# Kernel tuning notes

Measured on AMD Instinct MI355X. Metric: run time of the kernel, lower is better.

## Reference

```python
import jax, jax.numpy as jnp
import numpy as np

N_STATE = 2048
N_HEAD = 16
HEAD_DIM = N_STATE // N_HEAD  # 128
ROPE_THETA = 10000.0


def setup_inputs() -> dict:
    key = jax.random.key(0)
    ks = jax.random.split(key, 8)
    B, S, D = 2, 2048, N_STATE
    scale = 1.0 / np.sqrt(D)
    x = jax.random.normal(ks[0], (B, S, D), dtype=jnp.float32)
    Wq = jax.random.normal(ks[1], (D, D), dtype=jnp.float32) * scale
    bq = jnp.zeros((D,), dtype=jnp.float32)
    Wk = jax.random.normal(ks[2], (D, D), dtype=jnp.float32) * scale  # key has no bias
    Wv = jax.random.normal(ks[3], (D, D), dtype=jnp.float32) * scale
    bv = jnp.zeros((D,), dtype=jnp.float32)
    Wo = jax.random.normal(ks[4], (D, D), dtype=jnp.float32) * scale
    bo = jnp.zeros((D,), dtype=jnp.float32)
    return {"x": x, "Wq": Wq, "bq": bq, "Wk": Wk, "Wv": Wv, "bv": bv, "Wo": Wo, "bo": bo}


def _rope(t, pos):
    # t: [B, S, H, hd]; torchtune-style interleaved rotary (pairs of adjacent dims)
    hd = t.shape[-1]
    inv_freq = 1.0 / (ROPE_THETA ** (jnp.arange(0, hd, 2, dtype=jnp.float32) / hd))  # [hd/2]
    ang = pos[:, None] * inv_freq[None, :]                    # [S, hd/2]
    cos = jnp.cos(ang)[None, :, None, :].astype(t.dtype)       # [1,S,1,hd/2]
    sin = jnp.sin(ang)[None, :, None, :].astype(t.dtype)
    t1 = t[..., 0::2]
    t2 = t[..., 1::2]
    rot = jnp.stack([t1 * cos - t2 * sin, t2 * cos + t1 * sin], axis=-1)
    return rot.reshape(t.shape)


def reference(x, Wq, bq, Wk, Wv, bv, Wo, bo):
    B, S, D = x.shape
    H, hd = N_HEAD, D // N_HEAD
    q = (x @ Wq.T + bq).reshape(B, S, H, hd)
    k = (x @ Wk.T).reshape(B, S, H, hd)
    v = (x @ Wv.T + bv).reshape(B, S, H, hd)
    pos = jnp.arange(S, dtype=jnp.float32)
    q = _rope(q, pos)
    k = _rope(k, pos)
    # [B,H,S,hd]
    q = q.transpose(0, 2, 1, 3)
    k = k.transpose(0, 2, 1, 3)
    v = v.transpose(0, 2, 1, 3)
    scale = 1.0 / jnp.sqrt(jnp.asarray(hd, dtype=x.dtype))
    scores = jnp.einsum('bhqd,bhkd->bhqk', q, k) * scale       # [B,H,S,S]
    causal = jnp.tril(jnp.ones((S, S), dtype=bool))
    scores = jnp.where(causal[None, None], scores, jnp.finfo(scores.dtype).min)
    probs = jax.nn.softmax(scores, axis=-1)
    a = jnp.einsum('bhqk,bhkd->bhqd', probs, v)                # [B,H,S,hd]
    a = a.transpose(0, 2, 1, 3).reshape(B, S, D)
    return a @ Wo.T + bo
```

## Files before the change

### kernel.cpp

```cpp
#include <hip/hip_runtime.h>
#include <stdint.h>

typedef float f32x4 __attribute__((ext_vector_type(4)));
typedef __bf16 bf16x8 __attribute__((ext_vector_type(8)));
typedef unsigned short us8 __attribute__((ext_vector_type(8)));
typedef unsigned short us4 __attribute__((ext_vector_type(4)));
typedef unsigned int u32;

#define MFMA16(A, B, C) __builtin_amdgcn_mfma_f32_16x16x32_bf16( \
    __builtin_bit_cast(bf16x8, (A)), __builtin_bit_cast(bf16x8, (B)), (C), 0, 0, 0)

__device__ __forceinline__ unsigned short f2bf(float f) {
  u32 u = __builtin_bit_cast(u32, f);
  u = u + 0x7fffu + ((u >> 16) & 1u);
  return (unsigned short)(u >> 16);
}
__device__ __forceinline__ float bf2f(unsigned short b) {
  u32 u = ((u32)b) << 16;
  return __builtin_bit_cast(float, u);
}
__device__ __forceinline__ void gload16(const void* g, void* lds) {
  __builtin_amdgcn_global_load_lds((const __attribute__((address_space(1))) u32*)g,
                                   (__attribute__((address_space(3))) u32*)lds, 16, 0, 0);
}

__global__ __launch_bounds__(256) void convert_all(
    const float* __restrict__ x, const float* __restrict__ wq, const float* __restrict__ wk,
    const float* __restrict__ wv, const float* __restrict__ wo,
    unsigned short* __restrict__ xb, unsigned short* __restrict__ wcat,
    unsigned short* __restrict__ wob, float2* __restrict__ tab) {
  if (blockIdx.x >= 2048) {
    int t0 = ((int)blockIdx.x - 2048) * 2048 + (int)threadIdx.x * 8;
#pragma unroll
    for (int j = 0; j < 8; ++j) {
      int idx = t0 + j;
      int s = idx >> 6, i = idx & 63;
      float ang = (float)s * exp2f(-(float)i * 0.2076205059304703f);
      float sv, cv;
      sincosf(ang, &sv, &cv);
      tab[idx] = make_float2(cv, sv);
    }
    return;
  }
  int tid = blockIdx.x * 256 + threadIdx.x;
  int nth = 2048 * 256;
  const float* srcs[5] = {x, wq, wk, wv, wo};
  unsigned short* dsts[5] = {xb, wcat, wcat + 4194304, wcat + 8388608, wob};
  const int n4s[5] = {2097152, 1048576, 1048576, 1048576, 1048576};
#pragma unroll
  for (int sg = 0; sg < 5; ++sg) {
    const float4* s = (const float4*)srcs[sg];
    us4* d = (us4*)dsts[sg];
    int n4 = n4s[sg];
    for (int i = tid; i < n4; i += nth) {
      float4 v = s[i];
      us4 o;
      o[0] = f2bf(v.x); o[1] = f2bf(v.y); o[2] = f2bf(v.z); o[3] = f2bf(v.w);
      d[i] = o;
    }
  }
}

template <int EPI>
__global__ __launch_bounds__(512, 2) void gemmsw(
    const unsigned short* __restrict__ A, const unsigned short* __restrict__ B,
    int nTN, int N,
    float* __restrict__ outF, const float* __restrict__ bias,
    unsigned short* __restrict__ qb, unsigned short* __restrict__ kb,
    unsigned short* __restrict__ vtb, const float* __restrict__ bq,
    const float* __restrict__ bv, const float2* __restrict__ tab) {
  constexpr int KT = 32;
  __shared__ alignas(16) char L[131072];
  char* Lp = L;
  int bid = (int)blockIdx.x, nwg = (int)gridDim.x;
  {
    int qq = nwg >> 3;
    int xcd = bid & 7, idx = bid >> 3;
    bid = xcd * qq + idx;
  }
  int tm = bid / nTN, tn = bid % nTN;
  int t = (int)threadIdx.x, l = t & 63, w = t >> 6;
  int g = l >> 4, ln = l & 15;
  int wr = w >> 2, wc = w & 3;
  int lr = l >> 3, lc = l & 7;
  int scol = lc ^ lr;
  const unsigned short* pAs = A + (size_t)(tm * 256 + w * 8 + lr) * 2048 + scol * 8;
  const unsigned short* pBs = B + (size_t)(tn * 256 + w * 8 + lr) * 2048 + scol * 8;

  f32x4 acc[2][2][4][2] = {};
  us8 af[4][2], bf[2][2][2];

#define FENCE asm volatile("" ::: "memory")
#define BAR do { FENCE; __builtin_amdgcn_s_barrier(); FENCE; } while (0)
#define VMW_(n) asm volatile("s_waitcnt vmcnt(" #n ")" ::: "memory")
#define VMW(n) VMW_(n)
#define STA(i, kt, bufsel) do { if ((kt) < KT)                                \
    gload16(pAs + (size_t)(i) * 131072 + (size_t)(kt) * 64,                   \
            Lp + (bufsel) * 65536 + (i) * 8192 + w * 1024); } while (0)
#define STB(i, kt, bufsel) do { if ((kt) < KT)                                \
    gload16(pBs + (size_t)(i) * 131072 + (size_t)(kt) * 64,                   \
            Lp + (bufsel) * 65536 + 32768 + (i) * 8192 + w * 1024); } while (0)
#define RD_A(mh_, bufsel) do {                                                \
    _Pragma("unroll") for (int mf = 0; mf < 4; ++mf)                          \
    _Pragma("unroll") for (int kc = 0; kc < 2; ++kc)                          \
      af[mf][kc] = *(const us8*)(Lp + (bufsel) * 65536 +                      \
          (wr * 128 + (mh_) * 64 + mf * 16 + ln) * 128 +                      \
          ((kc * 64 + g * 16) ^ ((ln & 7) << 4)));                            \
  } while (0)
#define RD_B(nh_, bufsel) do {                                                \
    _Pragma("unroll") for (int nf = 0; nf < 2; ++nf)                          \
    _Pragma("unroll") for (int kc = 0; kc < 2; ++kc)                          \
      bf[nh_][nf][kc] = *(const us8*)(Lp + (bufsel) * 65536 + 32768 +         \
          (wc * 64 + (nh_) * 32 + nf * 16 + ln) * 128 +                       \
          ((kc * 64 + g * 16) ^ ((ln & 7) << 4)));                            \
  } while (0)
#define MM(mh_, nh_) do {                                                     \
    __builtin_amdgcn_s_setprio(1);                                            \
    _Pragma("unroll") for (int mf = 0; mf < 4; ++mf)                          \
    _Pragma("unroll") for (int nf = 0; nf < 2; ++nf)                          \
    _Pragma("unroll") for (int kc = 0; kc < 2; ++kc)                          \
      acc[mh_][nh_][mf][nf] = MFMA16(af[mf][kc], bf[nh_][nf][kc],             \
                                     acc[mh_][nh_][mf][nf]);                  \
    __builtin_amdgcn_s_setprio(0);                                            \
  } while (0)
#define TILE(kt, b, VM0, VM1, VM3) do {                                       \
   RD_A(0, b); RD_B(0, b);                                             \
          STB(0, (kt) + 1, (b) ^ 1); STB(1, (kt) + 1, (b) ^ 1);               \
          BAR; MM(0, 0); VMW(VM0); BAR;                                       \
   RD_B(1, b);                                                         \
          STA(0, (kt) + 1, (b) ^ 1); STA(2, (kt) + 1, (b) ^ 1);               \
          BAR; MM(0, 1); VMW(VM1); BAR;                                       \
   RD_A(1, b);                                                         \
          STB(2, (kt) + 1, (b) ^ 1); STB(3, (kt) + 1, (b) ^ 1);               \
          BAR; MM(1, 0); BAR;                                                 \
   STA(1, (kt) + 1, (b) ^ 1); STA(3, (kt) + 1, (b) ^ 1);               \
          MM(1, 1); VMW(VM3); BAR;                                            \
} while (0)

  STB(0, 0, 0); STB(1, 0, 0); STA(0, 0, 0); STA(2, 0, 0);
  STB(2, 0, 0); STB(3, 0, 0); STA(1, 0, 0); STA(3, 0, 0);
  VMW(4); BAR;

#pragma unroll 1
  for (int kt = 0; kt < 30; kt += 2) {
    TILE(kt, 0, 4, 4, 4);
    TILE(kt + 1, 1, 4, 4, 4);
  }
  TILE(30, 0, 4, 4, 4);
  TILE(31, 1, 2, 0, 0);

#undef TILE
#undef MM
#undef RD_B
#undef RD_A
#undef STB
#undef STA
#undef VMW
#undef VMW_
#undef BAR
#undef FENCE

  if (EPI == 1) {
#pragma unroll
    for (int mh = 0; mh < 2; ++mh)
#pragma unroll
    for (int nh = 0; nh < 2; ++nh)
#pragma unroll
    for (int mf = 0; mf < 4; ++mf)
#pragma unroll
    for (int nf = 0; nf < 2; ++nf) {
      int n = tn * 256 + wc * 64 + nh * 32 + nf * 16 + ln;
      float bz = bias[n];
      int m0 = tm * 256 + wr * 128 + mh * 64 + mf * 16 + g * 4;
#pragma unroll
      for (int r = 0; r < 4; ++r)
        outF[(size_t)(m0 + r) * N + n] = acc[mh][nh][mf][nf][r] + bz;
    }
  } else {
#pragma unroll
    for (int mh = 0; mh < 2; ++mh)
#pragma unroll
    for (int nh = 0; nh < 2; ++nh)
#pragma unroll
    for (int mf = 0; mf < 4; ++mf)
#pragma unroll
    for (int nf = 0; nf < 2; ++nf) {
      int n6 = tn * 256 + wc * 64 + nh * 32 + nf * 16 + ln;
      int sel = n6 >> 11, d = n6 & 2047, h = d >> 7, hd = d & 127;
      int m0 = tm * 256 + wr * 128 + mh * 64 + mf * 16 + g * 4;
      int b = m0 >> 11, s0 = m0 & 2047;
      if (sel == 2) {
        float badd = bv[d];
        us4 pk;
#pragma unroll
        for (int r = 0; r < 4; ++r) pk[r] = f2bf(acc[mh][nh][mf][nf][r] + badd);
        *(us4*)&vtb[((size_t)(b * 16 + h) * 128 + hd) * 2048 + s0] = pk;
      } else {
        unsigned short* dst = sel ? kb : qb;
        float badd = sel ? 0.f : bq[d];
        int odd = hd & 1;
#pragma unroll
        for (int r = 0; r < 4; ++r) {
          float val = acc[mh][nh][mf][nf][r] + badd;
          float pv = __shfl_xor(val, 1);
          float2 cs = tab[((s0 + r) << 6) | (hd >> 1)];
          float rot = odd ? (val * cs.x + pv * cs.y) : (val * cs.x - pv * cs.y);
          dst[((size_t)(b * 16 + h) * 2048 + (s0 + r)) * 128 + hd] = f2bf(rot);
        }
      }
    }
  }
}

template <int EPI>
__global__ __launch_bounds__(512, 2) void gemm2(
    const unsigned short* __restrict__ A, const unsigned short* __restrict__ B,
    int nTN, int N,
    float* __restrict__ outF, const float* __restrict__ bias) {
  constexpr int K = 2048, KT = 64;
  __shared__ alignas(16) char L[4 * 24576];
  int bid = (int)blockIdx.x, nwg = (int)gridDim.x;
  {
    int qq = nwg >> 3;
    int xcd = bid & 7, idx = bid >> 3;
    bid = xcd * qq + idx;
  }
  int tm = bid / nTN, tn = bid % nTN;
  int t = (int)threadIdx.x, l = t & 63, w = t >> 6;
  int g = l >> 4, ln = l & 15;
  int wr = w >> 2, wc = w & 3;
  const unsigned short* Ab =
      A + (size_t)(tm * 128 + w * 16 + (l >> 2)) * K + (((l & 3) ^ ((l >> 4) & 3))) * 8;
  const unsigned short* Bb =
      B + (size_t)(tn * 256 + w * 16 + (l >> 2)) * K + (((l & 3) ^ ((l >> 4) & 3))) * 8;
  f32x4 acc[4][4] = {};

#define STAGE(tile) do {                                                      \
    char* Lb = L + ((tile) & 3) * 24576 + w * 1024;                           \
    int kc = (tile) * 32;                                                     \
    gload16(Ab + kc, Lb);                                                     \
    gload16(Bb + kc, Lb + 8192);                                              \
    gload16(Bb + (size_t)128 * K + kc, Lb + 16384);                           \
  } while (0)

#define GITER(kt, VM) do {                                                    \
    asm volatile("s_waitcnt vmcnt(" #VM ")" ::: "memory");                    \
    __builtin_amdgcn_s_barrier();                                             \
    __builtin_amdgcn_sched_barrier(0);                                        \
    asm volatile("" ::: "memory");                                            \
    if ((kt) + 3 < KT) STAGE((kt) + 3);                                       \
    const unsigned short* Lc = (const unsigned short*)(L + ((kt) & 3) * 24576); \
    us8 af[4], bfr[4];                                                        \
    _Pragma("unroll") for (int mf = 0; mf < 4; ++mf)                          \
      af[mf] = *(const us8*)&Lc[(wr * 64 + mf * 16 + ln) * 32 +               \
                                ((g ^ ((ln >> 2) & 3)) * 8)];                 \
    _Pragma("unroll") for (int nf = 0; nf < 4; ++nf)                          \
      bfr[nf] = *(const us8*)&Lc[4096 + (wc * 64 + nf * 16 + ln) * 32 +       \
                                 ((g ^ ((ln >> 2) & 3)) * 8)];                \
    __builtin_amdgcn_s_setprio(1);                                            \
    _Pragma("unroll") for (int mf = 0; mf < 4; ++mf)                          \
      _Pragma("unroll") for (int nf = 0; nf < 4; ++nf)                        \
        acc[mf][nf] = MFMA16(af[mf], bfr[nf], acc[mf][nf]);                   \
    __builtin_amdgcn_s_setprio(0);                                            \
  } while (0)

  STAGE(0); STAGE(1); STAGE(2);
#pragma unroll 1
  for (int kt = 0; kt < KT - 2; ++kt) GITER(kt, 6);
  GITER(KT - 2, 3);
  GITER(KT - 1, 0);
#undef STAGE
#undef GITER

#pragma unroll
  for (int mf = 0; mf < 4; ++mf)
#pragma unroll
    for (int nf = 0; nf < 4; ++nf) {
      int n = tn * 256 + wc * 64 + nf * 16 + ln;
      float bz = bias[n];
#pragma unroll
      for (int r = 0; r < 4; ++r) {
        int m = tm * 128 + wr * 64 + mf * 16 + g * 4 + r;
        outF[(size_t)m * N + n] = acc[mf][nf][r] + bz;
      }
    }
}

__global__ __launch_bounds__(512) void attn_k(
    const unsigned short* __restrict__ qg, const unsigned short* __restrict__ kg,
    const unsigned short* __restrict__ vtg, unsigned short* __restrict__ ab) {
  __shared__ alignas(16) unsigned short Kl[2][64 * 128];
  __shared__ alignas(16) unsigned short Vl[2][128 * 64];
  __shared__ alignas(16) unsigned short Pl[8][16 * 72];
  int bh = (int)blockIdx.x & 31;
  int pr = (int)blockIdx.x >> 5;
  int t = (int)threadIdx.x, l = t & 63, w = t >> 6;
  int g = l >> 4, ln = l & 15;
  int b = bh >> 4, h = bh & 15;
  const size_t bq0 = (size_t)bh * 2048 * 128;

  const int qbA = pr * 128, qbB = (15 - pr) * 128;
  const int qrowA = qbA + w * 16 + ln, qrowB = qbB + w * 16 + ln;
  us8 qfA[4], qfB[4];
#pragma unroll
  for (int kf = 0; kf < 4; ++kf) {
    qfA[kf] = *(const us8*)&qg[bq0 + (size_t)qrowA * 128 + kf * 32 + g * 8];
    qfB[kf] = *(const us8*)&qg[bq0 + (size_t)qrowB * 128 + kf * 32 + g * 8];
  }
  f32x4 oA[8] = {}, oB[8] = {};
  float mA = -1e30f, lA = 0.f, mB = -1e30f, lB = 0.f;
  const int nktA = (qbA >> 6) + 2;
  const int nkt  = (qbB >> 6) + 2;

#define STAGEKV(kt1, bsel) do {                                               \
    _Pragma("unroll") for (int i = 0; i < 2; ++i) {                           \
      int fb = i * 8192 + w * 1024;                                           \
      int flat = fb + l * 16;                                                 \
      int row = flat >> 8, colb = flat & 255;                                 \
      int sc = colb ^ ((row & 7) << 4);                                       \
      gload16(kg + (bq0 + (size_t)((kt1) * 64 + row) * 128 + (sc >> 1)),      \
              (char*)Kl + (bsel) * 16384 + fb);                               \
      int rv = flat >> 7, cv2 = flat & 127;                                   \
      int scv = cv2 ^ ((rv & 7) << 4);                                        \
      gload16(vtg + (bq0 + (size_t)rv * 2048 + (kt1) * 64 + (scv >> 1)),      \
              (char*)Vl + (bsel) * 16384 + fb);                               \
    }                                                                         \
  } while (0)

#define COMPUTE(qf, o, mrow, lrow, qrow, kt, bo) do {                         \
    f32x4 st[4];                                                              \
    _Pragma("unroll") for (int kfr = 0; kfr < 4; ++kfr) {                     \
      f32x4 acc = {};                                                         \
      int row = kfr * 16 + ln;                                                \
      int swz = (row & 7) << 4;                                               \
      _Pragma("unroll") for (int kf = 0; kf < 4; ++kf) {                      \
        us8 kfrag = *(const us8*)((const char*)Kl + (bo) + row * 256 +        \
                                  ((kf * 64 + g * 16) ^ swz));                \
        acc = MFMA16(kfrag, qf[kf], acc);                                     \
      }                                                                       \
      st[kfr] = acc;                                                          \
    }                                                                         \
    float pmax = -1e30f;                                                      \
    _Pragma("unroll") for (int kfr = 0; kfr < 4; ++kfr)                       \
    _Pragma("unroll") for (int r = 0; r < 4; ++r) {                           \
      int key = (kt) * 64 + kfr * 16 + g * 4 + r;                             \
      float sv = key <= (qrow) ? st[kfr][r] * 0.08838834764831845f : -1e30f;  \
      st[kfr][r] = sv;                                                        \
      pmax = fmaxf(pmax, sv);                                                 \
    }                                                                         \
    pmax = fmaxf(pmax, __shfl_xor(pmax, 16));                                 \
    pmax = fmaxf(pmax, __shfl_xor(pmax, 32));                                 \
    if (__ballot(pmax > (mrow) + 8.f)) {                                      \
      float mnew = pmax > (mrow) + 8.f ? pmax : (mrow);                       \
      float corr = exp2f(((mrow) - mnew) * 1.44269504f);                      \
      (mrow) = mnew;                                                          \
      (lrow) *= corr;                                                         \
      _Pragma("unroll") for (int r = 0; r < 4; ++r) {                         \
        float cr = __shfl(corr, g * 4 + r);                                   \
        _Pragma("unroll") for (int nf = 0; nf < 8; ++nf) o[nf][r] *= cr;      \
      }                                                                       \
    }                                                                         \
    float lsum = 0.f;                                                         \
    _Pragma("unroll") for (int kfr = 0; kfr < 4; ++kfr) {                     \
      us4 pk;                                                                 \
      _Pragma("unroll") for (int r = 0; r < 4; ++r) {                         \
        float p = exp2f((st[kfr][r] - (mrow)) * 1.44269504f);                 \
        lsum += p;                                                            \
        pk[r] = f2bf(p);                                                      \
      }                                                                       \
      *(us4*)&Pl[w][ln * 72 + kfr * 16 + g * 4] = pk;                         \
    }                                                                         \
    lsum += __shfl_xor(lsum, 16);                                             \
    lsum += __shfl_xor(lsum, 32);                                             \
    (lrow) += lsum;                                                           \
    _Pragma("unroll") for (int kf2 = 0; kf2 < 2; ++kf2) {                     \
      us8 pa = *(const us8*)&Pl[w][ln * 72 + kf2 * 32 + g * 8];               \
      _Pragma("unroll") for (int nf = 0; nf < 8; ++nf) {                      \
        int row = nf * 16 + ln;                                               \
        us8 vb = *(const us8*)((const char*)Vl + (bo) + row * 128 +           \
                               ((kf2 * 64 + g * 16) ^ ((row & 7) << 4)));     \
        o[nf] = MFMA16(pa, vb, o[nf]);                                        \
      }                                                                       \
    }                                                                         \
  } while (0)

  STAGEKV(0, 0);
#pragma unroll 1
  for (int kt = 0; kt < nkt; ++kt) {
    __syncthreads();
    if (kt + 1 < nkt) STAGEKV(kt + 1, (kt + 1) & 1);
    int bo = (kt & 1) * 16384;
    COMPUTE(qfB, oB, mB, lB, qrowB, kt, bo);
    if (kt < nktA) COMPUTE(qfA, oA, mA, lA, qrowA, kt, bo);
  }
#undef COMPUTE
#undef STAGEKV

  {
    float invl = 1.f / lB;
#pragma unroll
    for (int r = 0; r < 4; ++r) {
      float ir = __shfl(invl, g * 4 + r);
      int srow = qbB + w * 16 + g * 4 + r;
      size_t base = ((size_t)b * 2048 + srow) * 2048 + h * 128 + ln;
#pragma unroll
      for (int nf = 0; nf < 8; ++nf) ab[base + (size_t)nf * 16] = f2bf(oB[nf][r] * ir);
    }
  }
  {
    float invl = 1.f / lA;
#pragma unroll
    for (int r = 0; r < 4; ++r) {
      float ir = __shfl(invl, g * 4 + r);
      int srow = qbA + w * 16 + g * 4 + r;
      size_t base = ((size_t)b * 2048 + srow) * 2048 + h * 128 + ln;
#pragma unroll
      for (int nf = 0; nf < 8; ++nf) ab[base + (size_t)nf * 16] = f2bf(oA[nf][r] * ir);
    }
  }
}

extern "C" void kernel_launch(void* const* d_in, const int* in_sizes, int n_in,
                              void* d_out, int out_size, void* d_ws, size_t ws_size,
                              hipStream_t stream) {
  const float* x  = (const float*)d_in[0];
  const float* Wq = (const float*)d_in[1];
  const float* bq = (const float*)d_in[2];
  const float* Wk = (const float*)d_in[3];
  const float* Wv = (const float*)d_in[4];
  const float* bv = (const float*)d_in[5];
  const float* Wo = (const float*)d_in[6];
  const float* bo = (const float*)d_in[7];
  float* out = (float*)d_out;

  unsigned short* ws = (unsigned short*)d_ws;
  unsigned short* xb   = ws;
  unsigned short* wcat = xb + 8388608;
  unsigned short* wob  = wcat + 12582912;
  unsigned short* qb   = wob + 4194304;
  unsigned short* kb   = qb + 8388608;
  unsigned short* vtb  = kb + 8388608;
  float2* tab = (float2*)(vtb + 8388608);

  convert_all<<<2112, 256, 0, stream>>>(x, Wq, Wk, Wv, Wo, xb, wcat, wob, tab);
  gemmsw<0><<<384, 512, 0, stream>>>(xb, wcat, 24, 6144,
                                     nullptr, nullptr, qb, kb, vtb, bq, bv, tab);
  attn_k<<<256, 512, 0, stream>>>(qb, kb, vtb, xb );
  gemm2<1><<<256, 512, 0, stream>>>(xb, wob, 8, 2048, out, bo);
}
```

Measured before the change: 266.3 us.

## Retile QKV projection GEMM to 256x192 tiles with 512 workgroups

The fused QKV GEMM tile changes from 256x256 to 256x192. The grid grows from 384 to 512 workgroups, which divides evenly across the 256 CUs instead of leaving a partial second wave, and LDS per block drops to 112KB. The inner loop is restructured: all A fragments are loaded once per k-tile, then three N-slices are streamed through with a new load/barrier/waitcnt schedule. The trade-off is lower arithmetic intensity per tile, more total A traffic, and a hand-tuned vmcnt schedule that must stay correct.

```diff
diff --git a/kernel.cpp b/kernel.cpp
--- a/kernel.cpp
+++ b/kernel.cpp
@@ -70,7 +70,7 @@
     unsigned short* __restrict__ vtb, const float* __restrict__ bq,
     const float* __restrict__ bv, const float2* __restrict__ tab) {
   constexpr int KT = 32;
-  __shared__ alignas(16) char L[131072];
+  __shared__ alignas(16) char L[114688];
   char* Lp = L;
   int bid = (int)blockIdx.x, nwg = (int)gridDim.x;
   {
@@ -85,10 +85,10 @@
   int lr = l >> 3, lc = l & 7;
   int scol = lc ^ lr;
   const unsigned short* pAs = A + (size_t)(tm * 256 + w * 8 + lr) * 2048 + scol * 8;
-  const unsigned short* pBs = B + (size_t)(tn * 256 + w * 8 + lr) * 2048 + scol * 8;
-
-  f32x4 acc[2][2][4][2] = {};
-  us8 af[4][2], bf[2][2][2];
+  const unsigned short* pBs = B + (size_t)(tn * 192 + w * 8 + lr) * 2048 + scol * 8;
+
+  f32x4 acc[2][3][4] = {};
+  us8 af[2][4][2], bf[2];
 
 #define FENCE asm volatile("" ::: "memory")
 #define BAR do { FENCE; __builtin_amdgcn_s_barrier(); FENCE; } while (0)
@@ -96,63 +96,62 @@
 #define VMW(n) VMW_(n)
 #define STA(i, kt, bufsel) do { if ((kt) < KT)                                \
     gload16(pAs + (size_t)(i) * 131072 + (size_t)(kt) * 64,                   \
-            Lp + (bufsel) * 65536 + (i) * 8192 + w * 1024); } while (0)
+            Lp + (bufsel) * 57344 + (i) * 8192 + w * 1024); } while (0)
 #define STB(i, kt, bufsel) do { if ((kt) < KT)                                \
     gload16(pBs + (size_t)(i) * 131072 + (size_t)(kt) * 64,                   \
-            Lp + (bufsel) * 65536 + 32768 + (i) * 8192 + w * 1024); } while (0)
-#define RD_A(mh_, bufsel) do {                                                \
+            Lp + (bufsel) * 57344 + 32768 + (i) * 8192 + w * 1024); } while (0)
+#define RD_AALL(bufsel) do {                                                  \
+    _Pragma("unroll") for (int mh = 0; mh < 2; ++mh)                          \
     _Pragma("unroll") for (int mf = 0; mf < 4; ++mf)                          \
     _Pragma("unroll") for (int kc = 0; kc < 2; ++kc)                          \
-      af[mf][kc] = *(const us8*)(Lp + (bufsel) * 65536 +                      \
-          (wr * 128 + (mh_) * 64 + mf * 16 + ln) * 128 +                      \
+      af[mh][mf][kc] = *(const us8*)(Lp + (bufsel) * 57344 +                  \
+          (wr * 128 + mh * 64 + mf * 16 + ln) * 128 +                         \
           ((kc * 64 + g * 16) ^ ((ln & 7) << 4)));                            \
   } while (0)
 #define RD_B(nh_, bufsel) do {                                                \
-    _Pragma("unroll") for (int nf = 0; nf < 2; ++nf)                          \
     _Pragma("unroll") for (int kc = 0; kc < 2; ++kc)                          \
-      bf[nh_][nf][kc] = *(const us8*)(Lp + (bufsel) * 65536 + 32768 +         \
-          (wc * 64 + (nh_) * 32 + nf * 16 + ln) * 128 +                       \
+      bf[kc] = *(const us8*)(Lp + (bufsel) * 57344 + 32768 +                  \
+          ((nh_) * 64 + wc * 16 + ln) * 128 +                                 \
           ((kc * 64 + g * 16) ^ ((ln & 7) << 4)));                            \
   } while (0)
-#define MM(mh_, nh_) do {                                                     \
+#define MMF(nh_) do {                                                         \
     __builtin_amdgcn_s_setprio(1);                                            \
+    _Pragma("unroll") for (int kc = 0; kc < 2; ++kc)                          \
+    _Pragma("unroll") for (int mh = 0; mh < 2; ++mh)                          \
     _Pragma("unroll") for (int mf = 0; mf < 4; ++mf)                          \
-    _Pragma("unroll") for (int nf = 0; nf < 2; ++nf)                          \
-    _Pragma("unroll") for (int kc = 0; kc < 2; ++kc)                          \
-      acc[mh_][nh_][mf][nf] = MFMA16(af[mf][kc], bf[nh_][nf][kc],             \
-                                     acc[mh_][nh_][mf][nf]);                  \
+      acc[mh][nh_][mf] = MFMA16(af[mh][mf][kc], bf[kc], acc[mh][nh_][mf]);    \
     __builtin_amdgcn_s_setprio(0);                                            \
   } while (0)
-#define TILE(kt, b, VM0, VM1, VM3) do {                                       \
-   RD_A(0, b); RD_B(0, b);                                             \
-          STB(0, (kt) + 1, (b) ^ 1); STB(1, (kt) + 1, (b) ^ 1);               \
-          BAR; MM(0, 0); VMW(VM0); BAR;                                       \
+#define TILE(kt, b, VM0, VM1, VMB) do {                                       \
+   RD_AALL(b); RD_B(0, b);                                             \
+          STA(0, (kt) + 1, (b) ^ 1); STA(1, (kt) + 1, (b) ^ 1);               \
+          STA(2, (kt) + 1, (b) ^ 1); STA(3, (kt) + 1, (b) ^ 1);               \
+          STB(0, (kt) + 1, (b) ^ 1);                                          \
+          BAR; MMF(0); VMW(VM0); BAR;                                         \
    RD_B(1, b);                                                         \
-          STA(0, (kt) + 1, (b) ^ 1); STA(2, (kt) + 1, (b) ^ 1);               \
-          BAR; MM(0, 1); VMW(VM1); BAR;                                       \
-   RD_A(1, b);                                                         \
-          STB(2, (kt) + 1, (b) ^ 1); STB(3, (kt) + 1, (b) ^ 1);               \
-          BAR; MM(1, 0); BAR;                                                 \
-   STA(1, (kt) + 1, (b) ^ 1); STA(3, (kt) + 1, (b) ^ 1);               \
-          MM(1, 1); VMW(VM3); BAR;                                            \
+          STB(1, (kt) + 1, (b) ^ 1);                                          \
+          BAR; MMF(1); VMW(VM1); BAR;                                         \
+   RD_B(2, b);                                                         \
+          STB(2, (kt) + 1, (b) ^ 1);                                          \
+          MMF(2); VMW(VMB); BAR;                                              \
 } while (0)
 
-  STB(0, 0, 0); STB(1, 0, 0); STA(0, 0, 0); STA(2, 0, 0);
-  STB(2, 0, 0); STB(3, 0, 0); STA(1, 0, 0); STA(3, 0, 0);
-  VMW(4); BAR;
+  STA(0, 0, 0); STA(1, 0, 0); STA(2, 0, 0); STA(3, 0, 0); STB(0, 0, 0);
+  STB(1, 0, 0); STB(2, 0, 0);
+  VMW(2); BAR;
 
 #pragma unroll 1
   for (int kt = 0; kt < 30; kt += 2) {
-    TILE(kt, 0, 4, 4, 4);
-    TILE(kt + 1, 1, 4, 4, 4);
-  }
-  TILE(30, 0, 4, 4, 4);
-  TILE(31, 1, 2, 0, 0);
+    TILE(kt, 0, 6, 6, 2);
+    TILE(kt + 1, 1, 6, 6, 2);
+  }
+  TILE(30, 0, 6, 6, 2);
+  TILE(31, 1, 1, 0, 0);
 
 #undef TILE
-#undef MM
+#undef MMF
 #undef RD_B
-#undef RD_A
+#undef RD_AALL
 #undef STB
 #undef STA
 #undef VMW
@@ -164,28 +163,24 @@
 #pragma unroll
     for (int mh = 0; mh < 2; ++mh)
 #pragma unroll
-    for (int nh = 0; nh < 2; ++nh)
-#pragma unroll
-    for (int mf = 0; mf < 4; ++mf)
-#pragma unroll
-    for (int nf = 0; nf < 2; ++nf) {
-      int n = tn * 256 + wc * 64 + nh * 32 + nf * 16 + ln;
+    for (int nh = 0; nh < 3; ++nh)
+#pragma unroll
+    for (int mf = 0; mf < 4; ++mf) {
+      int n = tn * 192 + nh * 64 + wc * 16 + ln;
       float bz = bias[n];
       int m0 = tm * 256 + wr * 128 + mh * 64 + mf * 16 + g * 4;
 #pragma unroll
       for (int r = 0; r < 4; ++r)
-        outF[(size_t)(m0 + r) * N + n] = acc[mh][nh][mf][nf][r] + bz;
+        outF[(size_t)(m0 + r) * N + n] = acc[mh][nh][mf][r] + bz;
     }
   } else {
 #pragma unroll
     for (int mh = 0; mh < 2; ++mh)
 #pragma unroll
-    for (int nh = 0; nh < 2; ++nh)
-#pragma unroll
-    for (int mf = 0; mf < 4; ++mf)
-#pragma unroll
-    for (int nf = 0; nf < 2; ++nf) {
-      int n6 = tn * 256 + wc * 64 + nh * 32 + nf * 16 + ln;
+    for (int nh = 0; nh < 3; ++nh)
+#pragma unroll
+    for (int mf = 0; mf < 4; ++mf) {
+      int n6 = tn * 192 + nh * 64 + wc * 16 + ln;
       int sel = n6 >> 11, d = n6 & 2047, h = d >> 7, hd = d & 127;
       int m0 = tm * 256 + wr * 128 + mh * 64 + mf * 16 + g * 4;
       int b = m0 >> 11, s0 = m0 & 2047;
@@ -193,7 +188,7 @@
         float badd = bv[d];
         us4 pk;
 #pragma unroll
-        for (int r = 0; r < 4; ++r) pk[r] = f2bf(acc[mh][nh][mf][nf][r] + badd);
+        for (int r = 0; r < 4; ++r) pk[r] = f2bf(acc[mh][nh][mf][r] + badd);
         *(us4*)&vtb[((size_t)(b * 16 + h) * 128 + hd) * 2048 + s0] = pk;
       } else {
         unsigned short* dst = sel ? kb : qb;
@@ -201,7 +196,7 @@
         int odd = hd & 1;
 #pragma unroll
         for (int r = 0; r < 4; ++r) {
-          float val = acc[mh][nh][mf][nf][r] + badd;
+          float val = acc[mh][nh][mf][r] + badd;
           float pv = __shfl_xor(val, 1);
           float2 cs = tab[((s0 + r) << 6) | (hd >> 1)];
           float rot = odd ? (val * cs.x + pv * cs.y) : (val * cs.x - pv * cs.y);
@@ -443,7 +438,7 @@
   float2* tab = (float2*)(vtb + 8388608);
 
   convert_all<<<2112, 256, 0, stream>>>(x, Wq, Wk, Wv, Wo, xb, wcat, wob, tab);
-  gemmsw<0><<<384, 512, 0, stream>>>(xb, wcat, 24, 6144,
+  gemmsw<0><<<512, 512, 0, stream>>>(xb, wcat, 32, 6144,
                                      nullptr, nullptr, qb, kb, vtb, bq, bv, tab);
   attn_k<<<256, 512, 0, stream>>>(qb, kb, vtb, xb );
   gemm2<1><<<256, 512, 0, stream>>>(xb, wob, 8, 2048, out, bo);
```

New measurement: 252.2 us. -5.3%, faster.
